# Optimization experiments

Hardware: AMD Instinct MI355X
Metric: run time of the kernel (lower is better)

## Reference

```python
import jax, jax.numpy as jnp
import numpy as np

N_NODES = 50000


def _gcn_conv(x, W, b, edge_index, num_nodes):
    # PyG GCNConv defaults: add self loops, symmetric normalization.
    h = x @ W  # [N, out]
    loop = jnp.arange(num_nodes, dtype=edge_index.dtype)
    src = jnp.concatenate([edge_index[0], loop])  # [E+N]
    dst = jnp.concatenate([edge_index[1], loop])
    ones = jnp.ones(src.shape[0], dtype=x.dtype)
    deg = jax.ops.segment_sum(ones, dst, num_segments=num_nodes)  # in-degree incl. self loop
    dinv = jnp.where(deg > 0, jax.lax.rsqrt(deg), 0.0)
    norm = dinv[src] * dinv[dst]  # [E+N]
    msgs = h[src] * norm[:, None]  # gather + scale (memory-bound)
    out = jax.ops.segment_sum(msgs, dst, num_segments=num_nodes)
    return out + b


def setup_inputs() -> dict:
    key = jax.random.key(0)
    k1, k2, k3, k4 = jax.random.split(key, 4)
    F_in, H = 128, 16
    x = jax.random.normal(k1, (N_NODES, F_in), dtype=jnp.float32)
    edge_index = jax.random.randint(k2, (2, 800000), 0, N_NODES, dtype=jnp.int64)
    # Glorot-ish init for weights
    W1 = jax.random.normal(k3, (F_in, H), dtype=jnp.float32) / np.sqrt(F_in)
    W2 = jax.random.normal(k4, (H, F_in), dtype=jnp.float32) / np.sqrt(H)
    b1 = jnp.zeros((H,), dtype=jnp.float32)
    b2 = jnp.zeros((F_in,), dtype=jnp.float32)
    return {"x": x, "edge_index": edge_index, "W1": W1, "b1": b1, "W2": W2, "b2": b2}


def reference(x, edge_index, W1, b1, W2, b2):
    h = jax.nn.relu(_gcn_conv(x, W1, b1, edge_index, N_NODES))
    out = _gcn_conv(h, W2, b2, edge_index, N_NODES)
    return out
```

## Files before the change

### kernel.cpp

```cpp
#include <hip/hip_runtime.h>

#define N_NODES 50000
#define NPB 128
#define NBUCKET ((N_NODES + NPB - 1) / NPB)
#define CAP 2816
#define CHUNK 2048
#define EPT 4


__global__ __launch_bounds__(512) void k_part(const int* __restrict__ src,
                                              const int* __restrict__ dst,
                                              int* __restrict__ gcursor,
                                              int* __restrict__ ewords, int E) {
    __shared__ int words[CHUNK];
    __shared__ int hist[512];
    __shared__ int lstart[512];
    __shared__ int gbase[512];
    __shared__ int wsum[8];

    int tid = threadIdx.x;
    int cbase = blockIdx.x * CHUNK;
    int count = min(CHUNK, E - cbase);

    hist[tid] = 0;
    __syncthreads();

    int w[EPT];
    if (cbase + CHUNK <= E) {
        int4 s4 = ((const int4*)(src + cbase))[tid];
        int4 d4 = ((const int4*)(dst + cbase))[tid];
        int ss[EPT] = {s4.x, s4.y, s4.z, s4.w};
        int dd[EPT] = {d4.x, d4.y, d4.z, d4.w};
#pragma unroll
        for (int r = 0; r < EPT; r++) {
            int b = dd[r] >> 7;
            w[r] = ss[r] | ((dd[r] & 127) << 16) | (b << 23);
            atomicAdd(&hist[b], 1);
        }
    } else {
#pragma unroll
        for (int r = 0; r < EPT; r++) {
            int i = tid * EPT + r;
            if (i < count) {
                int s = src[cbase + i];
                int d = dst[cbase + i];
                int b = d >> 7;
                w[r] = s | ((d & 127) << 16) | (b << 23);
                atomicAdd(&hist[b], 1);
            } else {
                w[r] = -1;
            }
        }
    }
    __syncthreads();

    int h = hist[tid];
    int lane = tid & 63;
    int v = h;
#pragma unroll
    for (int off = 1; off < 64; off <<= 1) {
        int t = __shfl_up(v, off, 64);
        if (lane >= off) v += t;
    }
    if (lane == 63) wsum[tid >> 6] = v;
    __syncthreads();
    int woff = 0;
    int wv = tid >> 6;
    for (int i = 0; i < wv; i++) woff += wsum[i];
    int excl = v + woff - h;
    hist[tid] = excl;
    lstart[tid] = excl;
    __syncthreads();

#pragma unroll
    for (int r = 0; r < EPT; r++) {
        if (w[r] != -1) {
            int b = ((unsigned)w[r]) >> 23;
            int pos = atomicAdd(&hist[b], 1);
            words[pos] = w[r];
        }
    }
    __syncthreads();

    if (tid < NBUCKET) {
        int nb = hist[tid] - lstart[tid];
        gbase[tid] = (nb > 0) ? atomicAdd(&gcursor[tid], nb) : 0;
    }
    __syncthreads();

    for (int i = tid; i < count; i += 512) {
        int ww = words[i];
        int b = ((unsigned)ww) >> 23;
        ewords[b * CAP + gbase[b] + (i - lstart[b])] = ww;
    }
}


__global__ __launch_bounds__(256) void k_sortgemm1(const int* __restrict__ ewords,
                                                   const int* __restrict__ gcursor,
                                                   unsigned short* __restrict__ eidx,
                                                   int* __restrict__ row_start,
                                                   int* __restrict__ deg,
                                                   float* __restrict__ dinv,
                                                   const float* __restrict__ x,
                                                   const float* __restrict__ W1,
                                                   float* __restrict__ h1) {
    __shared__ __align__(16) char smem[16 * 132 * 4 * 2];
    int tid = threadIdx.x;

    if (blockIdx.x < NBUCKET) {
        unsigned short* sorted = (unsigned short*)smem;
        int* hist = (int*)(smem + 5632);
        int* sc   = (int*)(smem + 5632 + 512);

        int b = blockIdx.x;
        int base = b * CAP;
        int count = gcursor[b];

        if (tid < NPB) hist[tid] = 0;
        __syncthreads();

        int w[(CAP + 255) / 256];
#pragma unroll
        for (int r = 0; r < (CAP + 255) / 256; r++) {
            int i = tid + 256 * r;
            if (i < count) {
                int ww = ewords[base + i];
                w[r] = ww;
                atomicAdd(&hist[(ww >> 16) & 127], 1);
            } else {
                w[r] = -1;
            }
        }
        __syncthreads();

        int v = 0;
        if (tid < NPB) { v = hist[tid]; sc[tid] = v; }
        __syncthreads();
        for (int off = 1; off < NPB; off <<= 1) {
            int t = 0;
            if (tid < NPB && tid >= off) t = sc[tid - off];
            __syncthreads();
            if (tid < NPB) sc[tid] += t;
            __syncthreads();
        }
        if (tid < NPB) {
            int excl = sc[tid] - v;
            int node = b * NPB + tid;
            if (node < N_NODES) {
                row_start[node] = base + excl;
                deg[node] = v;
                dinv[node] = rsqrtf((float)(v + 1));
            }
            hist[tid] = excl;
        }
        __syncthreads();

#pragma unroll
        for (int r = 0; r < (CAP + 255) / 256; r++) {
            if (w[r] != -1) {
                int ldst = (w[r] >> 16) & 127;
                int pos = atomicAdd(&hist[ldst], 1);
                sorted[pos] = (unsigned short)(w[r] & 0xFFFF);
            }
        }
        __syncthreads();

        for (int i = tid; i < count; i += 256) eidx[base + i] = sorted[i];
    } else {
        float* sx  = (float*)smem;
        float* swT = sx + 16 * 132;
        int n0 = (blockIdx.x - NBUCKET) * 16;

#pragma unroll
        for (int r = 0; r < 2; r++) {
            int q = tid + 256 * r;
            float4 v = ((const float4*)W1)[q];
            int k = q >> 2;
            int j4 = (q & 3) << 2;
            swT[(j4 + 0) * 132 + k] = v.x;
            swT[(j4 + 1) * 132 + k] = v.y;
            swT[(j4 + 2) * 132 + k] = v.z;
            swT[(j4 + 3) * 132 + k] = v.w;
        }
        const float4* x4 = (const float4*)(x + (size_t)n0 * 128);
#pragma unroll
        for (int r = 0; r < 2; r++) {
            int q = tid + 256 * r;
            float4 v = x4[q];
            int node = q >> 5;
            int k = (q & 31) << 2;
            *(float4*)&sx[node * 132 + k] = v;
        }
        __syncthreads();

        int node = tid >> 4;
        int j = tid & 15;
        float acc = 0.f;
#pragma unroll
        for (int k = 0; k < 128; k += 4) {
            float4 a = *(const float4*)&sx[node * 132 + k];
            float4 bb = *(const float4*)&swT[j * 132 + k];
            acc = fmaf(a.x, bb.x, acc);
            acc = fmaf(a.y, bb.y, acc);
            acc = fmaf(a.z, bb.z, acc);
            acc = fmaf(a.w, bb.w, acc);
        }
        h1[(size_t)(n0 + node) * 16 + j] = acc;
    }
}


__global__ __launch_bounds__(256) void k_agg1(const float* __restrict__ h1,
                                              const int* __restrict__ row_start,
                                              const int* __restrict__ deg,
                                              const unsigned short* __restrict__ eidx,
                                              const float* __restrict__ dinv,
                                              const float* __restrict__ b1,
                                              float* __restrict__ z1s) {
    int lane = threadIdx.x & 63;
    int node = blockIdx.x * 4 + (threadIdx.x >> 6);
    int f = lane & 15;
    int sub = lane >> 4;

    int start = row_start[node];
    int d = deg[node];

    float a0 = 0.f, a1 = 0.f;
    int i = sub;
    for (; i + 4 < d; i += 8) {
        int s0 = eidx[start + i];
        int s1 = eidx[start + i + 4];
        float d0 = dinv[s0];
        float d1 = dinv[s1];
        a0 = fmaf(d0, h1[s0 * 16 + f], a0);
        a1 = fmaf(d1, h1[s1 * 16 + f], a1);
    }
    if (i < d) {
        int s = eidx[start + i];
        a0 = fmaf(dinv[s], h1[s * 16 + f], a0);
    }
    float acc = a0 + a1;

    acc += __shfl_xor(acc, 16, 64);
    acc += __shfl_xor(acc, 32, 64);

    float dv = dinv[node];
    acc = fmaf(dv, h1[node * 16 + f], acc);
    float z = fmaxf(fmaf(dv, acc, b1[f]), 0.f);
    if (sub == 0) z1s[node * 16 + f] = dv * z;
}


__global__ __launch_bounds__(256) void k_aggmm(const float* __restrict__ z1s,
                                               const int* __restrict__ row_start,
                                               const int* __restrict__ deg,
                                               const unsigned short* __restrict__ eidx,
                                               const float* __restrict__ dinv,
                                               const float* __restrict__ W2,
                                               const float* __restrict__ b2,
                                               float* __restrict__ out) {
    __shared__ float sw2[16 * 128];
    __shared__ float sb2[128];
    int tid = threadIdx.x;

    ((float4*)sw2)[tid] = ((const float4*)W2)[tid];
    ((float4*)sw2)[tid + 256] = ((const float4*)W2)[tid + 256];
    if (tid < 32) ((float4*)sb2)[tid] = ((const float4*)b2)[tid];
    __syncthreads();

    int wave = tid >> 6;
    int lane = tid & 63;
    int f = lane & 15;
    int sub = lane >> 4;
    int nbase = (blockIdx.x * 4 + wave) * 16;

#pragma unroll 1
    for (int t = 0; t < 16; t++) {
        int node = nbase + t;
        if (node >= N_NODES) break;

        int start = row_start[node];
        int d = deg[node];

        float a0 = 0.f, a1 = 0.f;
        int i = sub;
        for (; i + 4 < d; i += 8) {
            int s0 = eidx[start + i];
            int s1 = eidx[start + i + 4];
            a0 += z1s[s0 * 16 + f];
            a1 += z1s[s1 * 16 + f];
        }
        if (i < d) a0 += z1s[(int)eidx[start + i] * 16 + f];
        float acc = a0 + a1;

        acc += __shfl_xor(acc, 16, 64);
        acc += __shfl_xor(acc, 32, 64);
        acc += z1s[node * 16 + f];
        float s2 = dinv[node] * acc;

        float o0 = sb2[lane];
        float o1 = sb2[lane + 64];
#pragma unroll
        for (int k = 0; k < 16; k++) {
            float sk = __shfl(s2, k, 64);
            o0 = fmaf(sk, sw2[k * 128 + lane], o0);
            o1 = fmaf(sk, sw2[k * 128 + 64 + lane], o1);
        }
        out[(size_t)node * 128 + lane] = o0;
        out[(size_t)node * 128 + 64 + lane] = o1;
    }
}


extern "C" void kernel_launch(void* const* d_in, const int* in_sizes, int n_in,
                              void* d_out, int out_size, void* d_ws, size_t ws_size,
                              hipStream_t stream) {
    const float* x  = (const float*)d_in[0];
    const int*   ei = (const int*)d_in[1];
    const float* W1 = (const float*)d_in[2];
    const float* b1 = (const float*)d_in[3];
    const float* W2 = (const float*)d_in[4];
    const float* b2 = (const float*)d_in[5];
    float* out = (float*)d_out;

    const int E = in_sizes[1] / 2;
    const int* src = ei;
    const int* dst = ei + E;

    char* ws = (char*)d_ws;
    int*            gcursor   = (int*)(ws + 0);
    int*            ewords    = (int*)(ws + 2048);
    float*          h1        = (float*)(ws + 4406272);
    unsigned short* eidx      = (unsigned short*)(ws + 7606272);
    int*            row_start = (int*)(ws + 9808384);
    int*            deg       = (int*)(ws + 10008384);
    float*          dinv      = (float*)(ws + 10208384);
    float*          z1s       = (float*)(ws + 10408384);

    const int NCHUNK = (E + CHUNK - 1) / CHUNK;

    hipMemsetAsync(gcursor, 0, NBUCKET * sizeof(int), stream);
    k_part<<<NCHUNK, 512, 0, stream>>>(src, dst, gcursor, ewords, E);
    k_sortgemm1<<<NBUCKET + N_NODES / 16, 256, 0, stream>>>(ewords, gcursor, eidx,
                                                            row_start, deg, dinv, x, W1, h1);
    k_agg1<<<N_NODES / 4, 256, 0, stream>>>(h1, row_start, deg, eidx, dinv, b1, z1s);
    k_aggmm<<<(N_NODES + 63) / 64, 256, 0, stream>>>(z1s, row_start, deg, eidx, dinv,
                                                     W2, b2, out);
}
```

Before: 169.5 us.

## Fuse partition with GEMM1, pre-scale h1 by dinv in sort, shuffle-broadcast edge indices

Moves the first dense GEMM into the partition kernel so both run in one launch, with CHUNK raised to 4096 and 8 edges per thread. The sort kernel now pre-multiplies h1 by dinv, which removes the per-edge dinv gather in the first aggregation. Both aggregation kernels load up to 64 neighbor indices cooperatively and broadcast them with shuffles instead of issuing per-edge index loads. k_aggmm also switches to a strided node assignment across 4 rounds. The risks are a hardcoded edge count in NCHUNK, the 12500 stride that assumes N_NODES is exactly 50000, and an extra read-modify-write pass over h1.

```diff
diff --git a/kernel.cpp b/kernel.cpp
--- a/kernel.cpp
+++ b/kernel.cpp
@@ -4,180 +4,116 @@
 #define NPB 128
 #define NBUCKET ((N_NODES + NPB - 1) / NPB)
 #define CAP 2816
-#define CHUNK 2048
-#define EPT 4
-
-
-__global__ __launch_bounds__(512) void k_part(const int* __restrict__ src,
-                                              const int* __restrict__ dst,
-                                              int* __restrict__ gcursor,
-                                              int* __restrict__ ewords, int E) {
-    __shared__ int words[CHUNK];
-    __shared__ int hist[512];
-    __shared__ int lstart[512];
-    __shared__ int gbase[512];
-    __shared__ int wsum[8];
-
-    int tid = threadIdx.x;
-    int cbase = blockIdx.x * CHUNK;
-    int count = min(CHUNK, E - cbase);
-
-    hist[tid] = 0;
-    __syncthreads();
-
-    int w[EPT];
-    if (cbase + CHUNK <= E) {
-        int4 s4 = ((const int4*)(src + cbase))[tid];
-        int4 d4 = ((const int4*)(dst + cbase))[tid];
-        int ss[EPT] = {s4.x, s4.y, s4.z, s4.w};
-        int dd[EPT] = {d4.x, d4.y, d4.z, d4.w};
-#pragma unroll
-        for (int r = 0; r < EPT; r++) {
-            int b = dd[r] >> 7;
-            w[r] = ss[r] | ((dd[r] & 127) << 16) | (b << 23);
-            atomicAdd(&hist[b], 1);
-        }
-    } else {
-#pragma unroll
-        for (int r = 0; r < EPT; r++) {
-            int i = tid * EPT + r;
-            if (i < count) {
-                int s = src[cbase + i];
-                int d = dst[cbase + i];
-                int b = d >> 7;
-                w[r] = s | ((d & 127) << 16) | (b << 23);
-                atomicAdd(&hist[b], 1);
-            } else {
-                w[r] = -1;
-            }
-        }
-    }
-    __syncthreads();
-
-    int h = hist[tid];
-    int lane = tid & 63;
-    int v = h;
-#pragma unroll
-    for (int off = 1; off < 64; off <<= 1) {
-        int t = __shfl_up(v, off, 64);
-        if (lane >= off) v += t;
-    }
-    if (lane == 63) wsum[tid >> 6] = v;
-    __syncthreads();
-    int woff = 0;
-    int wv = tid >> 6;
-    for (int i = 0; i < wv; i++) woff += wsum[i];
-    int excl = v + woff - h;
-    hist[tid] = excl;
-    lstart[tid] = excl;
-    __syncthreads();
-
-#pragma unroll
-    for (int r = 0; r < EPT; r++) {
-        if (w[r] != -1) {
-            int b = ((unsigned)w[r]) >> 23;
-            int pos = atomicAdd(&hist[b], 1);
-            words[pos] = w[r];
-        }
-    }
-    __syncthreads();
-
-    if (tid < NBUCKET) {
-        int nb = hist[tid] - lstart[tid];
-        gbase[tid] = (nb > 0) ? atomicAdd(&gcursor[tid], nb) : 0;
-    }
-    __syncthreads();
-
-    for (int i = tid; i < count; i += 512) {
-        int ww = words[i];
-        int b = ((unsigned)ww) >> 23;
-        ewords[b * CAP + gbase[b] + (i - lstart[b])] = ww;
-    }
-}
-
-
-__global__ __launch_bounds__(256) void k_sortgemm1(const int* __restrict__ ewords,
-                                                   const int* __restrict__ gcursor,
-                                                   unsigned short* __restrict__ eidx,
-                                                   int* __restrict__ row_start,
-                                                   int* __restrict__ deg,
-                                                   float* __restrict__ dinv,
+#define CHUNK 4096
+#define EPT 8
+#define G1_NPB 32
+#define NG1 ((N_NODES + G1_NPB - 1) / G1_NPB)
+#define NCHUNK ((800000 + CHUNK - 1) / CHUNK)
+
+
+__global__ __launch_bounds__(512) void k_partgemm1(const int* __restrict__ src,
+                                                   const int* __restrict__ dst,
+                                                   int* __restrict__ gcursor,
+                                                   int* __restrict__ ewords, int E,
                                                    const float* __restrict__ x,
                                                    const float* __restrict__ W1,
                                                    float* __restrict__ h1) {
-    __shared__ __align__(16) char smem[16 * 132 * 4 * 2];
+    __shared__ __align__(16) char smem[25344 + 64];
     int tid = threadIdx.x;
 
-    if (blockIdx.x < NBUCKET) {
-        unsigned short* sorted = (unsigned short*)smem;
-        int* hist = (int*)(smem + 5632);
-        int* sc   = (int*)(smem + 5632 + 512);
-
-        int b = blockIdx.x;
-        int base = b * CAP;
-        int count = gcursor[b];
-
-        if (tid < NPB) hist[tid] = 0;
-        __syncthreads();
-
-        int w[(CAP + 255) / 256];
-#pragma unroll
-        for (int r = 0; r < (CAP + 255) / 256; r++) {
-            int i = tid + 256 * r;
-            if (i < count) {
-                int ww = ewords[base + i];
-                w[r] = ww;
-                atomicAdd(&hist[(ww >> 16) & 127], 1);
-            } else {
-                w[r] = -1;
+    if (blockIdx.x < NCHUNK) {
+        int* words  = (int*)smem;
+        int* hist   = (int*)(smem + 16384);
+        int* lstart = (int*)(smem + 16384 + 2048);
+        int* gbase  = (int*)(smem + 16384 + 4096);
+        int* wsum   = (int*)(smem + 16384 + 6144);
+
+        int cbase = blockIdx.x * CHUNK;
+        int count = min(CHUNK, E - cbase);
+
+        hist[tid] = 0;
+        __syncthreads();
+
+        int w[EPT];
+        if (cbase + CHUNK <= E) {
+#pragma unroll
+            for (int hh = 0; hh < 2; hh++) {
+                int4 s4 = ((const int4*)(src + cbase))[tid + 512 * hh];
+                int4 d4 = ((const int4*)(dst + cbase))[tid + 512 * hh];
+                int ss[4] = {s4.x, s4.y, s4.z, s4.w};
+                int dd[4] = {d4.x, d4.y, d4.z, d4.w};
+#pragma unroll
+                for (int c = 0; c < 4; c++) {
+                    int b = dd[c] >> 7;
+                    w[hh * 4 + c] = ss[c] | ((dd[c] & 127) << 16) | (b << 23);
+                    atomicAdd(&hist[b], 1);
+                }
             }
-        }
-        __syncthreads();
-
-        int v = 0;
-        if (tid < NPB) { v = hist[tid]; sc[tid] = v; }
-        __syncthreads();
-        for (int off = 1; off < NPB; off <<= 1) {
-            int t = 0;
-            if (tid < NPB && tid >= off) t = sc[tid - off];
-            __syncthreads();
-            if (tid < NPB) sc[tid] += t;
-            __syncthreads();
-        }
-        if (tid < NPB) {
-            int excl = sc[tid] - v;
-            int node = b * NPB + tid;
-            if (node < N_NODES) {
-                row_start[node] = base + excl;
-                deg[node] = v;
-                dinv[node] = rsqrtf((float)(v + 1));
+        } else {
+#pragma unroll
+            for (int r = 0; r < EPT; r++) {
+                int i = tid * EPT + r;
+                if (i < count) {
+                    int s = src[cbase + i];
+                    int d = dst[cbase + i];
+                    int b = d >> 7;
+                    w[r] = s | ((d & 127) << 16) | (b << 23);
+                    atomicAdd(&hist[b], 1);
+                } else {
+                    w[r] = -1;
+                }
             }
-            hist[tid] = excl;
-        }
-        __syncthreads();
-
-#pragma unroll
-        for (int r = 0; r < (CAP + 255) / 256; r++) {
+        }
+        __syncthreads();
+
+        int h = hist[tid];
+        int lane = tid & 63;
+        int v = h;
+#pragma unroll
+        for (int off = 1; off < 64; off <<= 1) {
+            int t = __shfl_up(v, off, 64);
+            if (lane >= off) v += t;
+        }
+        if (lane == 63) wsum[tid >> 6] = v;
+        __syncthreads();
+        int woff = 0;
+        int wv = tid >> 6;
+        for (int i = 0; i < wv; i++) woff += wsum[i];
+        int excl = v + woff - h;
+        hist[tid] = excl;
+        lstart[tid] = excl;
+        __syncthreads();
+
+#pragma unroll
+        for (int r = 0; r < EPT; r++) {
             if (w[r] != -1) {
-                int ldst = (w[r] >> 16) & 127;
-                int pos = atomicAdd(&hist[ldst], 1);
-                sorted[pos] = (unsigned short)(w[r] & 0xFFFF);
+                int b = ((unsigned)w[r]) >> 23;
+                int pos = atomicAdd(&hist[b], 1);
+                words[pos] = w[r];
             }
         }
         __syncthreads();
 
-        for (int i = tid; i < count; i += 256) eidx[base + i] = sorted[i];
+        if (tid < NBUCKET) {
+            int nb = hist[tid] - lstart[tid];
+            gbase[tid] = (nb > 0) ? atomicAdd(&gcursor[tid], nb) : 0;
+        }
+        __syncthreads();
+
+        for (int i = tid; i < count; i += 512) {
+            int ww = words[i];
+            int b = ((unsigned)ww) >> 23;
+            ewords[b * CAP + gbase[b] + (i - lstart[b])] = ww;
+        }
     } else {
         float* sx  = (float*)smem;
-        float* swT = sx + 16 * 132;
-        int n0 = (blockIdx.x - NBUCKET) * 16;
-
-#pragma unroll
-        for (int r = 0; r < 2; r++) {
-            int q = tid + 256 * r;
-            float4 v = ((const float4*)W1)[q];
-            int k = q >> 2;
-            int j4 = (q & 3) << 2;
+        float* swT = sx + 32 * 132;
+        int n0 = (blockIdx.x - NCHUNK) * G1_NPB;
+
+        {
+            float4 v = ((const float4*)W1)[tid];
+            int k = tid >> 2;
+            int j4 = (tid & 3) << 2;
             swT[(j4 + 0) * 132 + k] = v.x;
             swT[(j4 + 1) * 132 + k] = v.y;
             swT[(j4 + 2) * 132 + k] = v.z;
@@ -186,11 +122,13 @@
         const float4* x4 = (const float4*)(x + (size_t)n0 * 128);
 #pragma unroll
         for (int r = 0; r < 2; r++) {
-            int q = tid + 256 * r;
-            float4 v = x4[q];
-            int node = q >> 5;
-            int k = (q & 31) << 2;
-            *(float4*)&sx[node * 132 + k] = v;
+            int q = tid + 512 * r;
+            int row = q >> 5;
+            if (n0 + row < N_NODES) {
+                float4 v = x4[q];
+                int k = (q & 31) << 2;
+                *(float4*)&sx[row * 132 + k] = v;
+            }
         }
         __syncthreads();
 
@@ -206,12 +144,97 @@
             acc = fmaf(a.z, bb.z, acc);
             acc = fmaf(a.w, bb.w, acc);
         }
-        h1[(size_t)(n0 + node) * 16 + j] = acc;
-    }
-}
-
-
-__global__ __launch_bounds__(256) void k_agg1(const float* __restrict__ h1,
+        int n = n0 + node;
+        if (n < N_NODES) h1[(size_t)n * 16 + j] = acc;
+    }
+}
+
+
+__global__ __launch_bounds__(256) void k_sortscale(const int* __restrict__ ewords,
+                                                   const int* __restrict__ gcursor,
+                                                   unsigned short* __restrict__ eidx,
+                                                   int* __restrict__ row_start,
+                                                   int* __restrict__ deg,
+                                                   float* __restrict__ dinv,
+                                                   float* __restrict__ h1) {
+    __shared__ unsigned short sorted[CAP];
+    __shared__ int hist[NPB];
+    __shared__ int sc[NPB];
+    __shared__ float sdinv[NPB];
+    int tid = threadIdx.x;
+    int b = blockIdx.x;
+    int base = b * CAP;
+    int count = gcursor[b];
+
+    if (tid < NPB) hist[tid] = 0;
+    __syncthreads();
+
+    int w[(CAP + 255) / 256];
+#pragma unroll
+    for (int r = 0; r < (CAP + 255) / 256; r++) {
+        int i = tid + 256 * r;
+        if (i < count) {
+            int ww = ewords[base + i];
+            w[r] = ww;
+            atomicAdd(&hist[(ww >> 16) & 127], 1);
+        } else {
+            w[r] = -1;
+        }
+    }
+    __syncthreads();
+
+    int v = 0;
+    if (tid < NPB) { v = hist[tid]; sc[tid] = v; }
+    __syncthreads();
+    for (int off = 1; off < NPB; off <<= 1) {
+        int t = 0;
+        if (tid < NPB && tid >= off) t = sc[tid - off];
+        __syncthreads();
+        if (tid < NPB) sc[tid] += t;
+        __syncthreads();
+    }
+    if (tid < NPB) {
+        int excl = sc[tid] - v;
+        int node = b * NPB + tid;
+        float dv = rsqrtf((float)(v + 1));
+        sdinv[tid] = dv;
+        if (node < N_NODES) {
+            row_start[node] = base + excl;
+            deg[node] = v;
+            dinv[node] = dv;
+        }
+        hist[tid] = excl;
+    }
+    __syncthreads();
+
+#pragma unroll
+    for (int r = 0; r < (CAP + 255) / 256; r++) {
+        if (w[r] != -1) {
+            int ldst = (w[r] >> 16) & 127;
+            int pos = atomicAdd(&hist[ldst], 1);
+            sorted[pos] = (unsigned short)(w[r] & 0xFFFF);
+        }
+    }
+    __syncthreads();
+
+    for (int i = tid; i < count; i += 256) eidx[base + i] = sorted[i];
+
+    float4* h4 = (float4*)(h1 + (size_t)b * NPB * 16);
+    int nvalid4 = (b == NBUCKET - 1) ? (N_NODES - b * NPB) * 4 : NPB * 4;
+#pragma unroll
+    for (int r = 0; r < 2; r++) {
+        int q = tid + 256 * r;
+        if (q < nvalid4) {
+            float dv = sdinv[q >> 2];
+            float4 vv = h4[q];
+            vv.x *= dv; vv.y *= dv; vv.z *= dv; vv.w *= dv;
+            h4[q] = vv;
+        }
+    }
+}
+
+
+__global__ __launch_bounds__(256) void k_agg1(const float* __restrict__ h1s,
                                               const int* __restrict__ row_start,
                                               const int* __restrict__ deg,
                                               const unsigned short* __restrict__ eidx,
@@ -225,28 +248,31 @@
 
     int start = row_start[node];
     int d = deg[node];
+    int m = min(d, 64);
+
+    int e = 0;
+    if (m > 0) e = (int)eidx[start + min(lane, m - 1)];
 
     float a0 = 0.f, a1 = 0.f;
+    int iters = (m + 7) >> 3;
     int i = sub;
-    for (; i + 4 < d; i += 8) {
-        int s0 = eidx[start + i];
-        int s1 = eidx[start + i + 4];
-        float d0 = dinv[s0];
-        float d1 = dinv[s1];
-        a0 = fmaf(d0, h1[s0 * 16 + f], a0);
-        a1 = fmaf(d1, h1[s1 * 16 + f], a1);
-    }
-    if (i < d) {
-        int s = eidx[start + i];
-        a0 = fmaf(dinv[s], h1[s * 16 + f], a0);
-    }
+    for (int t = 0; t < iters; t++, i += 8) {
+        int s0 = __shfl(e, min(i, m - 1), 64);
+        int s1 = __shfl(e, min(i + 4, m - 1), 64);
+        float v0 = h1s[s0 * 16 + f];
+        float v1 = h1s[s1 * 16 + f];
+        if (i < m) a0 += v0;
+        if (i + 4 < m) a1 += v1;
+    }
+    for (int q = 64 + sub; q < d; q += 4)
+        a0 += h1s[(int)eidx[start + q] * 16 + f];
     float acc = a0 + a1;
 
     acc += __shfl_xor(acc, 16, 64);
     acc += __shfl_xor(acc, 32, 64);
+    acc += h1s[node * 16 + f];
 
     float dv = dinv[node];
-    acc = fmaf(dv, h1[node * 16 + f], acc);
     float z = fmaxf(fmaf(dv, acc, b1[f]), 0.f);
     if (sub == 0) z1s[node * 16 + f] = dv * z;
 }
@@ -269,29 +295,35 @@
     if (tid < 32) ((float4*)sb2)[tid] = ((const float4*)b2)[tid];
     __syncthreads();
 
-    int wave = tid >> 6;
     int lane = tid & 63;
+    int gw = blockIdx.x * 4 + (tid >> 6);
     int f = lane & 15;
     int sub = lane >> 4;
-    int nbase = (blockIdx.x * 4 + wave) * 16;
 
 #pragma unroll 1
-    for (int t = 0; t < 16; t++) {
-        int node = nbase + t;
-        if (node >= N_NODES) break;
+    for (int t = 0; t < 4; t++) {
+        int node = gw + t * 12500;
 
         int start = row_start[node];
         int d = deg[node];
+        int m = min(d, 64);
+
+        int e = 0;
+        if (m > 0) e = (int)eidx[start + min(lane, m - 1)];
 
         float a0 = 0.f, a1 = 0.f;
+        int iters = (m + 7) >> 3;
         int i = sub;
-        for (; i + 4 < d; i += 8) {
-            int s0 = eidx[start + i];
-            int s1 = eidx[start + i + 4];
-            a0 += z1s[s0 * 16 + f];
-            a1 += z1s[s1 * 16 + f];
-        }
-        if (i < d) a0 += z1s[(int)eidx[start + i] * 16 + f];
+        for (int u = 0; u < iters; u++, i += 8) {
+            int s0 = __shfl(e, min(i, m - 1), 64);
+            int s1 = __shfl(e, min(i + 4, m - 1), 64);
+            float v0 = z1s[s0 * 16 + f];
+            float v1 = z1s[s1 * 16 + f];
+            if (i < m) a0 += v0;
+            if (i + 4 < m) a1 += v1;
+        }
+        for (int q = 64 + sub; q < d; q += 4)
+            a0 += z1s[(int)eidx[start + q] * 16 + f];
         float acc = a0 + a1;
 
         acc += __shfl_xor(acc, 16, 64);
@@ -338,13 +370,9 @@
     float*          dinv      = (float*)(ws + 10208384);
     float*          z1s       = (float*)(ws + 10408384);
 
-    const int NCHUNK = (E + CHUNK - 1) / CHUNK;
-
     hipMemsetAsync(gcursor, 0, NBUCKET * sizeof(int), stream);
-    k_part<<<NCHUNK, 512, 0, stream>>>(src, dst, gcursor, ewords, E);
-    k_sortgemm1<<<NBUCKET + N_NODES / 16, 256, 0, stream>>>(ewords, gcursor, eidx,
-                                                            row_start, deg, dinv, x, W1, h1);
+    k_partgemm1<<<NCHUNK + NG1, 512, 0, stream>>>(src, dst, gcursor, ewords, E, x, W1, h1);
+    k_sortscale<<<NBUCKET, 256, 0, stream>>>(ewords, gcursor, eidx, row_start, deg, dinv, h1);
     k_agg1<<<N_NODES / 4, 256, 0, stream>>>(h1, row_start, deg, eidx, dinv, b1, z1s);
-    k_aggmm<<<(N_NODES + 63) / 64, 256, 0, stream>>>(z1s, row_start, deg, eidx, dinv,
-                                                     W2, b2, out);
-}
+    k_aggmm<<<(N_NODES / 4) / 4, 256, 0, stream>>>(z1s, row_start, deg, eidx, dinv, W2, b2, out);
+}
```

Measured after the change: 153.6 us. 1.1x faster.
